# Kernel tuning notes

Measured on AMD Instinct MI355X. Metric: run time of the kernel, lower is better.

The kernel has to match this reference:

```python
import jax, jax.numpy as jnp
import numpy as np

B, T, N, D = 8, 192, 64, 512
H = 8
DH = D // H
C = 8


def setup_inputs() -> dict:
    key = jax.random.key(0)
    ks = jax.random.split(key, 10)
    s = 1.0 / np.sqrt(D)
    return {
        "x": jax.random.normal(ks[0], (B, T, N, D), dtype=jnp.float32),
        "Wq_w": jax.random.normal(ks[1], (D, D), dtype=jnp.float32) * s,
        "Wq_b": jnp.zeros((D,), dtype=jnp.float32),
        "Wv_w": jax.random.normal(ks[2], (D, D), dtype=jnp.float32) * s,
        "Wv_b": jnp.zeros((D,), dtype=jnp.float32),
        "Wk": jax.random.normal(ks[3], (C, D, D), dtype=jnp.float32) * s,
        "bk": jnp.zeros((C, D), dtype=jnp.float32),
        "proj_w": jax.random.normal(ks[4], (D, D), dtype=jnp.float32) * s,
        "proj_b": jnp.zeros((D,), dtype=jnp.float32),
        "cluster_ids": jax.random.randint(ks[5], (N,), 0, C, dtype=jnp.int64),
    }


def reference(x, Wq_w, Wq_b, Wv_w, Wv_b, Wk, bk, proj_w, proj_b, cluster_ids):
    # torch Linear: y = x @ W.T + b
    Q = jnp.einsum('btnd,ed->btne', x, Wq_w) + Wq_b
    V = jnp.einsum('btnd,ed->btne', x, Wv_w) + Wv_b
    # per-cluster K projection == per-node weight gather (grouped GEMM)
    Wk_n = Wk[cluster_ids]          # [N, D, D]
    bk_n = bk[cluster_ids]          # [N, D]
    K = jnp.einsum('btnd,nde->btne', x, Wk_n) + bk_n

    def split_heads(z):
        # [B,T,N,D] -> [B,N,H,T,DH]
        return z.reshape(B, T, N, H, DH).transpose(0, 2, 3, 1, 4)

    Qh, Kh, Vh = split_heads(Q), split_heads(K), split_heads(V)
    scores = jnp.einsum('bnhtd,bnhsd->bnhts', Qh, Kh) / np.sqrt(DH).astype(np.float32)
    attn = jax.nn.softmax(scores, axis=-1)
    out_h = jnp.einsum('bnhts,bnhsd->bnhtd', attn, Vh)
    out = out_h.transpose(0, 3, 1, 2, 4).reshape(B, T, N, D)
    return jnp.einsum('btnd,ed->btne', out, proj_w) + proj_b
```

## Files before the change

kernel.cpp:

```cpp
#include <hip/hip_runtime.h>
#include <hip/hip_bf16.h>

typedef __bf16 bf16x8 __attribute__((ext_vector_type(8)));
typedef float  f32x4  __attribute__((ext_vector_type(4)));

#define MFMA16(a, b, c) __builtin_amdgcn_mfma_f32_16x16x32_bf16(a, b, c, 0, 0, 0)

__device__ __forceinline__ void async16(const __bf16* g, __bf16* l) {
    __builtin_amdgcn_global_load_lds(
        (const __attribute__((address_space(1))) unsigned int*)g,
        (__attribute__((address_space(3))) unsigned int*)l, 16, 0, 0);
}


__global__ void k_cast3(const float* __restrict__ wq, const float* __restrict__ wv,
                        const float* __restrict__ wp,
                        __bf16* __restrict__ oq, __bf16* __restrict__ ov,
                        __bf16* __restrict__ op) {
    int i = blockIdx.x * 256 + threadIdx.x;
    oq[i] = (__bf16)wq[i];
    ov[i] = (__bf16)wv[i];
    op[i] = (__bf16)wp[i];
}

__global__ void k_twk(const float* __restrict__ wk, __bf16* __restrict__ o) {
    int i = blockIdx.x * 256 + threadIdx.x;
    int c = i >> 18;
    int r = i & 262143;
    int d = r >> 9;
    int e = r & 511;
    o[(c << 18) + (e << 9) + d] = (__bf16)wk[i];
}

__global__ void k_castx(const float* __restrict__ x, __bf16* __restrict__ o) {
    size_t i = ((size_t)blockIdx.x * 256 + threadIdx.x) * 8;
    float4 f0 = *(const float4*)(x + i);
    float4 f1 = *(const float4*)(x + i + 4);
    bf16x8 v;
    v[0] = (__bf16)f0.x; v[1] = (__bf16)f0.y; v[2] = (__bf16)f0.z; v[3] = (__bf16)f0.w;
    v[4] = (__bf16)f1.x; v[5] = (__bf16)f1.y; v[6] = (__bf16)f1.z; v[7] = (__bf16)f1.w;
    *(bf16x8*)(o + i) = v;
}

__launch_bounds__(512, 2)
__global__ void k_qkv(const __bf16* __restrict__ xb,
                      const __bf16* __restrict__ WqE, const __bf16* __restrict__ WvE,
                      const __bf16* __restrict__ WkE,
                      const float* __restrict__ bq, const float* __restrict__ bv,
                      const float* __restrict__ bk, const int* __restrict__ cid,
                      __bf16* __restrict__ Qw, __bf16* __restrict__ Kw,
                      __bf16* __restrict__ Vw) {
    const int g   = blockIdx.y * 36 + blockIdx.x;
    const int s   = (g & 7) * 288 + (g >> 3);
    const int n   = s / 36;
    const int r36 = s - n * 36;
    const int mx  = r36 / 6;
    const int ey  = r36 - mx * 6;
    const int m0  = mx * 256;
    const int e0  = ey * 256;
    const int seg  = e0 >> 9;
    const int eoff = e0 & 511;
    const int c    = cid[n];

    const __bf16* Wb = (seg == 0) ? WqE : (seg == 1) ? WvE : (WkE + ((size_t)c << 18));
    __bf16*       Ob = (seg == 0) ? Qw : (seg == 1) ? Vw : Kw;

    __shared__ __align__(16) __bf16 As[2][256 * 64];
    __shared__ __align__(16) __bf16 Bs[2][256 * 64];

    const int tid  = threadIdx.x;
    const int lane = tid & 63;
    const int w    = tid >> 6;
    const int wm2  = w >> 2;
    const int wn4  = w & 3;
    const int l15  = lane & 15, qd = lane >> 4;

    const int sr  = tid >> 3;
    const int sch = tid & 7;
    const int sw8 = (sch ^ (sr & 7)) * 8;
    const __bf16* aG = xb + ((size_t)(m0 + sr) * 64 + n) * 512 + sw8;
    const __bf16* bG = Wb + ((size_t)(eoff + sr) << 9) + sw8;
    const int ldst = tid * 8;

    const int co0  = (qd ^ (l15 & 7)) * 8;
    const int arow = wm2 * 128 + l15;
    const int brow = wn4 * 64 + l15;

    f32x4 acc[8][4];
#pragma unroll
    for (int i = 0; i < 8; ++i)
#pragma unroll
        for (int j = 0; j < 4; ++j) acc[i][j] = (f32x4){0.f, 0.f, 0.f, 0.f};

#pragma unroll
    for (int q = 0; q < 4; ++q) {
        async16(aG + (size_t)q * 2097152, &As[0][q * 4096 + ldst]);
        async16(bG + (size_t)q * 32768,   &Bs[0][q * 4096 + ldst]);
    }
    asm volatile("s_waitcnt vmcnt(0)" ::: "memory");
    __builtin_amdgcn_s_barrier();

    bf16x8 bfr[4][2];
    for (int kt = 0; kt < 8; ++kt) {
        const int cb = kt & 1, nb = cb ^ 1;
        const int kn = (kt + 1) * 64;
#pragma unroll
        for (int q = 0; q < 4; ++q) {
            if (q < 2 && kt < 7) {
#pragma unroll
                for (int h = 0; h < 2; ++h) {
                    const int sl = 2 * q + h;
                    async16(aG + (size_t)sl * 2097152 + kn, &As[nb][sl * 4096 + ldst]);
                    async16(bG + (size_t)sl * 32768 + kn,   &Bs[nb][sl * 4096 + ldst]);
                }
            }
            if (q == 0) {
#pragma unroll
                for (int j = 0; j < 4; ++j) {
                    bfr[j][0] = *(const bf16x8*)&Bs[cb][(brow + j * 16) * 64 + co0];
                    bfr[j][1] = *(const bf16x8*)&Bs[cb][(brow + j * 16) * 64 + (co0 ^ 32)];
                }
            }
            bf16x8 a00 = *(const bf16x8*)&As[cb][(arow + (2 * q) * 16) * 64 + co0];
            bf16x8 a01 = *(const bf16x8*)&As[cb][(arow + (2 * q) * 16) * 64 + (co0 ^ 32)];
            bf16x8 a10 = *(const bf16x8*)&As[cb][(arow + (2 * q + 1) * 16) * 64 + co0];
            bf16x8 a11 = *(const bf16x8*)&As[cb][(arow + (2 * q + 1) * 16) * 64 + (co0 ^ 32)];

            __builtin_amdgcn_s_barrier();
            asm volatile("s_waitcnt lgkmcnt(0)" ::: "memory");
            __builtin_amdgcn_sched_barrier(0);
            __builtin_amdgcn_s_setprio(1);
#pragma unroll
            for (int j = 0; j < 4; ++j) {
                acc[2 * q][j]     = MFMA16(a00, bfr[j][0], acc[2 * q][j]);
                acc[2 * q + 1][j] = MFMA16(a10, bfr[j][0], acc[2 * q + 1][j]);
            }
#pragma unroll
            for (int j = 0; j < 4; ++j) {
                acc[2 * q][j]     = MFMA16(a01, bfr[j][1], acc[2 * q][j]);
                acc[2 * q + 1][j] = MFMA16(a11, bfr[j][1], acc[2 * q + 1][j]);
            }
            __builtin_amdgcn_s_setprio(0);
            if (q == 3) asm volatile("s_waitcnt vmcnt(0)" ::: "memory");
            __builtin_amdgcn_s_barrier();
        }
    }

    float bias[4];
#pragma unroll
    for (int j = 0; j < 4; ++j) {
        int e = eoff + wn4 * 64 + j * 16 + l15;
        bias[j] = (seg == 0) ? bq[e] : (seg == 1) ? bv[e] : bk[(c << 9) + e];
    }
#pragma unroll
    for (int i = 0; i < 8; ++i) {
#pragma unroll
        for (int rx = 0; rx < 4; ++rx) {
            int m  = m0 + wm2 * 128 + i * 16 + qd * 4 + rx;
            int bb = m / 192;
            int tt = m - bb * 192;
            size_t ro = ((size_t)(bb * 64 + n) * 192 + tt) << 9;
#pragma unroll
            for (int j = 0; j < 4; ++j) {
                int e = eoff + wn4 * 64 + j * 16 + l15;
                Ob[ro + e] = (__bf16)(acc[i][j][rx] + bias[j]);
            }
        }
    }
}

__launch_bounds__(768)
__global__ void k_attn(const __bf16* __restrict__ Qw, const __bf16* __restrict__ Kw,
                       const __bf16* __restrict__ Vw, __bf16* __restrict__ Ow) {
    const int h = blockIdx.x, n = blockIdx.y, b = blockIdx.z;
    __shared__ __align__(16) __bf16 Ks[192 * 72];
    __shared__ __align__(16) __bf16 Vt[64 * 192];
    __shared__ __align__(16) __bf16 Ps[192 * 200];

    const int tid  = threadIdx.x;
    const int lane = tid & 63, w = tid >> 6;
    const int l15  = lane & 15, qd = lane >> 4;
    const size_t base = ((size_t)((b * 64 + n) * 192) << 9) + h * 64;

    for (int i = tid; i < 1536; i += 768) {
        int row = i >> 3, pp = i & 7;
        *(bf16x8*)&Ks[row * 72 + 8 * pp] =
            *(const bf16x8*)(Kw + base + ((size_t)row << 9) + 8 * pp);
    }
#pragma unroll
    for (int rr = 0; rr < 2; ++rr) {
        int idx = rr * 768 + tid;
        int e = idx & 63, sb = idx >> 6;
        bf16x8 v;
#pragma unroll
        for (int j = 0; j < 8; ++j)
            v[j] = Vw[base + (size_t)(sb * 8 + j) * 512 + e];
        *(bf16x8*)&Vt[e * 192 + ((sb ^ (e & 7)) * 8)] = v;
    }
    __syncthreads();

    const __bf16* qp = Qw + base + ((size_t)(16 * w + l15) << 9) + 8 * qd;
    bf16x8 aq0 = *(const bf16x8*)(qp);
    bf16x8 aq1 = *(const bf16x8*)(qp + 32);

    f32x4 S[12];
#pragma unroll
    for (int ct = 0; ct < 12; ++ct) {
        f32x4 acc = (f32x4){0.f, 0.f, 0.f, 0.f};
        bf16x8 b0 = *(const bf16x8*)&Ks[(16 * ct + l15) * 72 + 8 * qd];
        bf16x8 b1 = *(const bf16x8*)&Ks[(16 * ct + l15) * 72 + 32 + 8 * qd];
        acc = MFMA16(aq0, b0, acc);
        acc = MFMA16(aq1, b1, acc);
        S[ct] = acc;
    }

    float mx[4] = {-1e30f, -1e30f, -1e30f, -1e30f};
#pragma unroll
    for (int ct = 0; ct < 12; ++ct)
#pragma unroll
        for (int rx = 0; rx < 4; ++rx) mx[rx] = fmaxf(mx[rx], S[ct][rx]);
#pragma unroll
    for (int mk = 1; mk < 16; mk <<= 1)
#pragma unroll
        for (int rx = 0; rx < 4; ++rx) mx[rx] = fmaxf(mx[rx], __shfl_xor(mx[rx], mk, 64));

    const float sc = 0.125f * 1.44269504088896f;
    float sm[4] = {0.f, 0.f, 0.f, 0.f};
#pragma unroll
    for (int ct = 0; ct < 12; ++ct) {
#pragma unroll
        for (int rx = 0; rx < 4; ++rx) {
            float pe = exp2f((S[ct][rx] - mx[rx]) * sc);
            sm[rx] += pe;
            Ps[(w * 16 + qd * 4 + rx) * 200 + 16 * ct + l15] = (__bf16)pe;
        }
    }
#pragma unroll
    for (int mk = 1; mk < 16; mk <<= 1)
#pragma unroll
        for (int rx = 0; rx < 4; ++rx) sm[rx] += __shfl_xor(sm[rx], mk, 64);

    __syncthreads();

    float inv[4];
#pragma unroll
    for (int rx = 0; rx < 4; ++rx) inv[rx] = 1.f / sm[rx];

#pragma unroll
    for (int et = 0; et < 4; ++et) {
        f32x4 acc = (f32x4){0.f, 0.f, 0.f, 0.f};
#pragma unroll
        for (int sn = 0; sn < 6; ++sn) {
            bf16x8 pa = *(const bf16x8*)&Ps[(w * 16 + l15) * 200 + sn * 32 + 8 * qd];
            bf16x8 vb = *(const bf16x8*)
                &Vt[(et * 16 + l15) * 192 + (((sn * 4 + qd) ^ (l15 & 7)) * 8)];
            acc = MFMA16(pa, vb, acc);
        }
#pragma unroll
        for (int rx = 0; rx < 4; ++rx) {
            int t = 16 * w + 4 * qd + rx;
            Ow[base + ((size_t)t << 9) + et * 16 + l15] = (__bf16)(acc[rx] * inv[rx]);
        }
    }
}

__launch_bounds__(256)
__global__ void k_proj(const __bf16* __restrict__ Ow, const __bf16* __restrict__ WpE,
                       const float* __restrict__ bp, float* __restrict__ out) {
    const int n  = blockIdx.z;
    const int m0 = blockIdx.x * 128;
    const int e0 = blockIdx.y * 128;
    __shared__ __align__(16) __bf16 As[128 * 64];
    __shared__ __align__(16) __bf16 Bs[128 * 64];

    const int tid  = threadIdx.x;
    const int lane = tid & 63, w = tid >> 6;
    const int wm   = w >> 1, wn = w & 1;
    const int l15  = lane & 15, qd = lane >> 4;
    const int lr   = lane >> 3, lc = lane & 7;
    const int sc8  = (lc ^ lr) * 8;
    const int sw   = l15 & 7;

    const __bf16* agj[4];
#pragma unroll
    for (int j = 0; j < 4; ++j) {
        int m  = m0 + w * 32 + j * 8 + lr;
        int bb = m / 192;
        int tt = m - bb * 192;
        agj[j] = Ow + (((size_t)(bb * 64 + n) * 192 + tt) << 9) + sc8;
    }
    __bf16* al = As + w * 2048 + lr * 64 + lc * 8;
    const __bf16* bg  = WpE + ((size_t)(e0 + w * 32 + lr) << 9) + sc8;
    __bf16*       blp = Bs + w * 2048 + lr * 64 + lc * 8;

    f32x4 acc[4][4];
#pragma unroll
    for (int i = 0; i < 4; ++i)
#pragma unroll
        for (int j = 0; j < 4; ++j) acc[i][j] = (f32x4){0.f, 0.f, 0.f, 0.f};

    for (int kk = 0; kk < 8; ++kk) {
        const int k0 = kk * 64;
        __syncthreads();
#pragma unroll
        for (int j = 0; j < 4; ++j) {
            async16(agj[j] + k0, al + j * 512);
            async16(bg + j * 4096 + k0, blp + j * 512);
        }
        __syncthreads();

#pragma unroll
        for (int kc = 0; kc < 2; ++kc) {
            const int co = ((kc * 4 + qd) ^ sw) * 8;
            bf16x8 a0 = *(const bf16x8*)&As[(wm * 64 + l15) * 64 + co];
            bf16x8 a1 = *(const bf16x8*)&As[(wm * 64 + 16 + l15) * 64 + co];
            bf16x8 a2 = *(const bf16x8*)&As[(wm * 64 + 32 + l15) * 64 + co];
            bf16x8 a3 = *(const bf16x8*)&As[(wm * 64 + 48 + l15) * 64 + co];
#pragma unroll
            for (int j = 0; j < 4; ++j) {
                bf16x8 fb = *(const bf16x8*)&Bs[(wn * 64 + j * 16 + l15) * 64 + co];
                acc[0][j] = MFMA16(a0, fb, acc[0][j]);
                acc[1][j] = MFMA16(a1, fb, acc[1][j]);
                acc[2][j] = MFMA16(a2, fb, acc[2][j]);
                acc[3][j] = MFMA16(a3, fb, acc[3][j]);
            }
        }
    }

    float bias[4];
#pragma unroll
    for (int j = 0; j < 4; ++j) bias[j] = bp[e0 + wn * 64 + j * 16 + l15];
#pragma unroll
    for (int i = 0; i < 4; ++i) {
#pragma unroll
        for (int rx = 0; rx < 4; ++rx) {
            int m = m0 + wm * 64 + i * 16 + qd * 4 + rx;
            size_t ro = ((size_t)(m * 64 + n)) << 9;
#pragma unroll
            for (int j = 0; j < 4; ++j) {
                int e = e0 + wn * 64 + j * 16 + l15;
                out[ro + e] = acc[i][j][rx] + bias[j];
            }
        }
    }
}

extern "C" void kernel_launch(void* const* d_in, const int* in_sizes, int n_in,
                              void* d_out, int out_size, void* d_ws, size_t ws_size,
                              hipStream_t stream) {
    const float* x    = (const float*)d_in[0];
    const float* Wq_w = (const float*)d_in[1];
    const float* Wq_b = (const float*)d_in[2];
    const float* Wv_w = (const float*)d_in[3];
    const float* Wv_b = (const float*)d_in[4];
    const float* Wk   = (const float*)d_in[5];
    const float* bk   = (const float*)d_in[6];
    const float* Wp   = (const float*)d_in[7];
    const float* bp   = (const float*)d_in[8];
    const int*   cid  = (const int*)d_in[9];
    float* out = (float*)d_out;

    __bf16* WqE = (__bf16*)d_ws;
    __bf16* WvE = WqE + (1 << 18);
    __bf16* WpE = WvE + (1 << 18);
    __bf16* WkE = WpE + (1 << 18);
    __bf16* Qw  = WkE + (8 << 18);
    __bf16* Kw  = Qw + 50331648LL;
    __bf16* Vw  = Kw + 50331648LL;
    __bf16* XO  = Vw + 50331648LL;

    k_cast3<<<1024, 256, 0, stream>>>(Wq_w, Wv_w, Wp, WqE, WvE, WpE);
    k_twk<<<8192, 256, 0, stream>>>(Wk, WkE);
    k_castx<<<24576, 256, 0, stream>>>(x, XO);
    k_qkv<<<dim3(36, 64), 512, 0, stream>>>(XO, WqE, WvE, WkE, Wq_b, Wv_b, bk, cid,
                                            Qw, Kw, Vw);
    k_attn<<<dim3(8, 64, 8), 768, 0, stream>>>(Qw, Kw, Vw, XO);
    k_proj<<<dim3(12, 4, 64), 256, 0, stream>>>(XO, WpE, bp, out);
}
```

Before: 862.0 us.

## Replace double-buffered K=64 tiles with four-stage K=32 async pipeline in QKV GEMM

The QKV projection GEMM now uses four LDS ring slots holding K=32 slices in place of two K=64 buffers. Async global-to-LDS loads run three stages ahead, gated by vmcnt counts, with one barrier per slice. This is meant to hide global load latency better and cut the per-quarter barriers of the old loop. The trade-offs are a new swizzle (XOR over 4 chunks, which may cause more LDS bank conflicts) and a more complex prologue and epilogue, with the same LDS footprint.

```diff
diff --git a/kernel.cpp b/kernel.cpp
--- a/kernel.cpp
+++ b/kernel.cpp
@@ -65,8 +65,8 @@
     const __bf16* Wb = (seg == 0) ? WqE : (seg == 1) ? WvE : (WkE + ((size_t)c << 18));
     __bf16*       Ob = (seg == 0) ? Qw : (seg == 1) ? Vw : Kw;
 
-    __shared__ __align__(16) __bf16 As[2][256 * 64];
-    __shared__ __align__(16) __bf16 Bs[2][256 * 64];
+    __shared__ __align__(16) __bf16 Ar[4][256 * 32];
+    __shared__ __align__(16) __bf16 Br[4][256 * 32];
 
     const int tid  = threadIdx.x;
     const int lane = tid & 63;
@@ -75,16 +75,17 @@
     const int wn4  = w & 3;
     const int l15  = lane & 15, qd = lane >> 4;
 
-    const int sr  = tid >> 3;
-    const int sch = tid & 7;
-    const int sw8 = (sch ^ (sr & 7)) * 8;
-    const __bf16* aG = xb + ((size_t)(m0 + sr) * 64 + n) * 512 + sw8;
-    const __bf16* bG = Wb + ((size_t)(eoff + sr) << 9) + sw8;
-    const int ldst = tid * 8;
-
-    const int co0  = (qd ^ (l15 & 7)) * 8;
-    const int arow = wm2 * 128 + l15;
-    const int brow = wn4 * 64 + l15;
+    const int sr  = tid >> 2;
+    const int sp  = tid & 3;
+    const int sch = (sp ^ (sr & 3)) * 8;
+    const __bf16* aG0 = xb + ((size_t)(m0 + sr) * 64 + n) * 512 + sch;
+    const __bf16* aG1 = aG0 + (size_t)128 * 64 * 512;
+    const __bf16* bG0 = Wb + ((size_t)(eoff + sr) << 9) + sch;
+    const __bf16* bG1 = bG0 + ((size_t)128 << 9);
+
+    const int cro   = (qd ^ (l15 & 3)) * 8;
+    const int arow0 = (wm2 * 128 + l15) * 32;
+    const int brow0 = (wn4 * 64 + l15) * 32;
 
     f32x4 acc[8][4];
 #pragma unroll
@@ -92,59 +93,58 @@
 #pragma unroll
         for (int j = 0; j < 4; ++j) acc[i][j] = (f32x4){0.f, 0.f, 0.f, 0.f};
 
-#pragma unroll
-    for (int q = 0; q < 4; ++q) {
-        async16(aG + (size_t)q * 2097152, &As[0][q * 4096 + ldst]);
-        async16(bG + (size_t)q * 32768,   &Bs[0][q * 4096 + ldst]);
-    }
+    auto issue = [&](int t) {
+        const int slot = t & 3;
+        const int k0 = t * 32;
+        __bf16* ad = &Ar[slot][tid * 8];
+        __bf16* bd = &Br[slot][tid * 8];
+        async16(aG0 + k0, ad);
+        async16(aG1 + k0, ad + 4096);
+        async16(bG0 + k0, bd);
+        async16(bG1 + k0, bd + 4096);
+    };
+    auto compute = [&](int slot) {
+        const __bf16* Asl = Ar[slot];
+        const __bf16* Bsl = Br[slot];
+        bf16x8 bfr[4], af[8];
+#pragma unroll
+        for (int j = 0; j < 4; ++j)
+            bfr[j] = *(const bf16x8*)&Bsl[brow0 + j * 512 + cro];
+#pragma unroll
+        for (int i = 0; i < 8; ++i)
+            af[i] = *(const bf16x8*)&Asl[arow0 + i * 512 + cro];
+        asm volatile("s_waitcnt lgkmcnt(0)" ::: "memory");
+        __builtin_amdgcn_sched_barrier(0);
+        __builtin_amdgcn_s_setprio(1);
+#pragma unroll
+        for (int i = 0; i < 8; ++i)
+#pragma unroll
+            for (int j = 0; j < 4; ++j)
+                acc[i][j] = MFMA16(af[i], bfr[j], acc[i][j]);
+        __builtin_amdgcn_s_setprio(0);
+    };
+
+    issue(0); issue(1); issue(2);
+    asm volatile("s_waitcnt vmcnt(8)" ::: "memory");
+    __builtin_amdgcn_s_barrier();
+    __builtin_amdgcn_sched_barrier(0);
+
+    for (int t = 0; t < 13; ++t) {
+        issue(t + 3);
+        compute(t & 3);
+        asm volatile("s_waitcnt vmcnt(8)" ::: "memory");
+        __builtin_amdgcn_s_barrier();
+        __builtin_amdgcn_sched_barrier(0);
+    }
+    compute(1);
+    asm volatile("s_waitcnt vmcnt(4)" ::: "memory");
+    __builtin_amdgcn_s_barrier();
+    __builtin_amdgcn_sched_barrier(0);
+    compute(2);
     asm volatile("s_waitcnt vmcnt(0)" ::: "memory");
     __builtin_amdgcn_s_barrier();
-
-    bf16x8 bfr[4][2];
-    for (int kt = 0; kt < 8; ++kt) {
-        const int cb = kt & 1, nb = cb ^ 1;
-        const int kn = (kt + 1) * 64;
-#pragma unroll
-        for (int q = 0; q < 4; ++q) {
-            if (q < 2 && kt < 7) {
-#pragma unroll
-                for (int h = 0; h < 2; ++h) {
-                    const int sl = 2 * q + h;
-                    async16(aG + (size_t)sl * 2097152 + kn, &As[nb][sl * 4096 + ldst]);
-                    async16(bG + (size_t)sl * 32768 + kn,   &Bs[nb][sl * 4096 + ldst]);
-                }
-            }
-            if (q == 0) {
-#pragma unroll
-                for (int j = 0; j < 4; ++j) {
-                    bfr[j][0] = *(const bf16x8*)&Bs[cb][(brow + j * 16) * 64 + co0];
-                    bfr[j][1] = *(const bf16x8*)&Bs[cb][(brow + j * 16) * 64 + (co0 ^ 32)];
-                }
-            }
-            bf16x8 a00 = *(const bf16x8*)&As[cb][(arow + (2 * q) * 16) * 64 + co0];
-            bf16x8 a01 = *(const bf16x8*)&As[cb][(arow + (2 * q) * 16) * 64 + (co0 ^ 32)];
-            bf16x8 a10 = *(const bf16x8*)&As[cb][(arow + (2 * q + 1) * 16) * 64 + co0];
-            bf16x8 a11 = *(const bf16x8*)&As[cb][(arow + (2 * q + 1) * 16) * 64 + (co0 ^ 32)];
-
-            __builtin_amdgcn_s_barrier();
-            asm volatile("s_waitcnt lgkmcnt(0)" ::: "memory");
-            __builtin_amdgcn_sched_barrier(0);
-            __builtin_amdgcn_s_setprio(1);
-#pragma unroll
-            for (int j = 0; j < 4; ++j) {
-                acc[2 * q][j]     = MFMA16(a00, bfr[j][0], acc[2 * q][j]);
-                acc[2 * q + 1][j] = MFMA16(a10, bfr[j][0], acc[2 * q + 1][j]);
-            }
-#pragma unroll
-            for (int j = 0; j < 4; ++j) {
-                acc[2 * q][j]     = MFMA16(a01, bfr[j][1], acc[2 * q][j]);
-                acc[2 * q + 1][j] = MFMA16(a11, bfr[j][1], acc[2 * q + 1][j]);
-            }
-            __builtin_amdgcn_s_setprio(0);
-            if (q == 3) asm volatile("s_waitcnt vmcnt(0)" ::: "memory");
-            __builtin_amdgcn_s_barrier();
-        }
-    }
+    __builtin_amdgcn_sched_barrier(0);
+    compute(3);
 
     float bias[4];
 #pragma unroll
```

Result: faster. 802.2 us (-6.9%).
